# Optimization experiments

Hardware: AMD Instinct MI355X
Metric: run time of the kernel (lower is better)

The kernel has to match this reference:

```python
import jax, jax.numpy as jnp
import numpy as np

N = 8192
IN_F = 512
OUT_F = 512
ALPHA = 0.2
NEG_BIG = -9.0e15


def setup_inputs() -> dict:
    key = jax.random.key(0)
    k1, k2, k3, k4 = jax.random.split(key, 4)
    adjacency = jax.random.randint(k1, (N, N), 0, 2, dtype=jnp.int32)
    features = jax.random.normal(k2, (N, IN_F), dtype=jnp.float32)
    # Linear weight stored as [in, out] (h = x @ W)
    W = jax.random.normal(k3, (IN_F, OUT_F), dtype=jnp.float32) * (1.0 / np.sqrt(IN_F))
    attn = jax.random.normal(k4, (2 * OUT_F, 1), dtype=jnp.float32) * 0.05
    return {"adjacency": adjacency, "features": features, "W": W, "attn": attn}


def reference(adjacency, features, W, attn):
    h = features @ W  # [N, F]
    # Additive decomposition of concat([h_i, h_j]) @ attn:
    # score_ij = a1 . h_i + a2 . h_j  (identical math, no NxNx2F tensor)
    a1 = attn[:OUT_F, 0]  # [F]
    a2 = attn[OUT_F:, 0]  # [F]
    s1 = h @ a1  # [N] contribution of source node i
    s2 = h @ a2  # [N] contribution of target node j
    e = jax.nn.leaky_relu(s1[:, None] + s2[None, :], negative_slope=ALPHA)  # [N, N]
    e = jnp.where(adjacency > 0, e, NEG_BIG)
    attention = jax.nn.softmax(e, axis=1)  # [N, N]
    h_prime = attention @ h  # [N, F]
    return jax.nn.elu(h_prime)
```

## Files before the change

kernel.cpp:

```cpp
#include <hip/hip_runtime.h>
#include <hip/hip_bf16.h>
#include <cstdint>

#define NN 8192
#define F 512
#define LOG2E 1.4426950408889634f

typedef __attribute__((ext_vector_type(8))) short bf16x8;
typedef __attribute__((ext_vector_type(4))) float f32x4;
typedef unsigned int uint32;
typedef unsigned long long u64;
typedef unsigned char uchar;

__device__ __forceinline__ short f2bf(float x){
  __hip_bfloat16 h = __float2bfloat16(x);
  return *reinterpret_cast<short*>(&h);
}

__global__ __launch_bounds__(256) void k_wa(const float* __restrict__ W, const float* __restrict__ attn,
                     float* __restrict__ wa){
  const int lane = threadIdx.x&63, wid = threadIdx.x>>6;
  const int id = blockIdx.x*4 + wid;
  const int b = id>>9, c = id&511;
  const float4* Wr = (const float4*)(W + (size_t)c*F);
  const float4* av = (const float4*)(attn + b*F);
  float s = 0.f;
  #pragma unroll
  for (int h=0;h<2;++h){
    const int k = lane + h*64;
    const float4 wv = Wr[k], a = av[k];
    s += wv.x*a.x + wv.y*a.y + wv.z*a.z + wv.w*a.w;
  }
  for (int off=32;off;off>>=1) s += __shfl_down(s,off);
  if (lane==0) wa[id] = s;
}

__global__ __launch_bounds__(256) void k_tw(const float* __restrict__ W, short* __restrict__ WbT){
  __shared__ short t[64][72];
  const int k0 = blockIdx.x*64, n0 = blockIdx.y*64;
  #pragma unroll
  for (int it=0;it<16;++it){
    const int idx = it*256 + threadIdx.x;
    const int r = idx>>6, c = idx&63;
    t[r][c] = f2bf(W[(size_t)(k0+r)*F + n0 + c]);
  }
  __syncthreads();
  #pragma unroll
  for (int it=0;it<2;++it){
    const int idx = it*256 + threadIdx.x;
    const int n = idx>>3, g = idx&7;
    short v[8];
    #pragma unroll
    for (int e=0;e<8;++e) v[e] = t[g*8+e][n];
    *(uint4*)(WbT + (size_t)(n0+n)*F + k0 + g*8) = *(const uint4*)v;
  }
}

__global__ __launch_bounds__(256) void k_prep(const float* __restrict__ X, const float* __restrict__ wa,
    short* __restrict__ Xb, float2* __restrict__ rowAB, uint32* __restrict__ uwb){
  const int lane = threadIdx.x&63, wid = threadIdx.x>>6;
  const int row = blockIdx.x*4 + wid;
  const float4* X4 = (const float4*)(X + (size_t)row*F);
  const float4* A4 = (const float4*)wa;
  const float4* B4 = (const float4*)(wa + F);
  uint2* Xb4 = (uint2*)(Xb + (size_t)row*F);
  float a1 = 0.f, a2 = 0.f;
  #pragma unroll
  for (int h=0;h<2;++h){
    const int c = lane + h*64;
    const float4 x = X4[c];
    const float4 a = A4[c];
    const float4 b = B4[c];
    a1 += x.x*a.x + x.y*a.y + x.z*a.z + x.w*a.w;
    a2 += x.x*b.x + x.y*b.y + x.z*b.z + x.w*b.w;
    short o[4] = {f2bf(x.x),f2bf(x.y),f2bf(x.z),f2bf(x.w)};
    Xb4[c] = *(const uint2*)o;
  }
  for (int off=32;off;off>>=1){ a1 += __shfl_down(a1,off); a2 += __shfl_down(a2,off); }
  if (lane==0){
    const float s1 = a1*LOG2E, s2 = a2*LOG2E;
    rowAB[row] = make_float2(exp2f(s1), exp2f(0.2f*s1));
    const float u = exp2f(s2), w = exp2f(0.2f*s2);
    uwb[row] = (uint32)(unsigned short)f2bf(u) | ((uint32)(unsigned short)f2bf(w)<<16);
  }
}

__global__ __launch_bounds__(256,2) void k_gemm1(const short* __restrict__ Xb,
    const short* __restrict__ WbT, short* __restrict__ HT){
  __shared__ char smem[33280];
  short* At = (short*)smem;
  short* Bt = (short*)(smem + 16384);
  const int tid=threadIdx.x, lane=tid&63, wid=tid>>6;
  const int m0 = blockIdx.x*128, n0 = blockIdx.y*128;
  f32x4 acc[2][8];
  #pragma unroll
  for (int a=0;a<2;++a)
    #pragma unroll
    for (int b=0;b<8;++b) acc[a][b] = (f32x4){0.f,0.f,0.f,0.f};

  for (int t=0;t<8;++t){
    const int k0 = t*64;
    __syncthreads();
    #pragma unroll
    for (int rnd=0;rnd<4;++rnd){
      const int s = rnd*256 + tid;
      const int n = s>>3, kc = s&7;
      uint4 va = *(const uint4*)(Xb  + (size_t)(m0+n)*F + k0 + kc*8);
      uint4 vb = *(const uint4*)(WbT + (size_t)(n0+n)*F + k0 + kc*8);
      const int off = n*128 + ((kc^(n&7))*16);
      *(uint4*)((char*)At + off) = va;
      *(uint4*)((char*)Bt + off) = vb;
    }
    __syncthreads();
    #pragma unroll
    for (int ks=0;ks<2;++ks){
      const int kc = ks*4 + (lane>>4);
      int r0 = wid*32 + (lane&15);
      int r1 = r0 + 16;
      bf16x8 af0 = *(const bf16x8*)((char*)At + r0*128 + ((kc^(r0&7))*16));
      bf16x8 af1 = *(const bf16x8*)((char*)At + r1*128 + ((kc^(r1&7))*16));
      #pragma unroll
      for (int nf=0;nf<8;++nf){
        const int c = nf*16 + (lane&15);
        bf16x8 bf = *(const bf16x8*)((char*)Bt + c*128 + ((kc^(c&7))*16));
        acc[0][nf] = __builtin_amdgcn_mfma_f32_16x16x32_bf16(af0, bf, acc[0][nf],0,0,0);
        acc[1][nf] = __builtin_amdgcn_mfma_f32_16x16x32_bf16(af1, bf, acc[1][nf],0,0,0);
      }
    }
  }
  __syncthreads();
  short* ct = (short*)smem;
  #pragma unroll
  for (int mf=0;mf<2;++mf)
    #pragma unroll
    for (int nf=0;nf<8;++nf)
      #pragma unroll
      for (int q=0;q<4;++q){
        int r = wid*32 + mf*16 + (lane>>4)*4 + q;
        int c = nf*16 + (lane&15);
        ct[r*130+c] = f2bf(acc[mf][nf][q]);
      }
  __syncthreads();
  {
    const int c = tid>>1, ih0 = (tid&1)*64;
    #pragma unroll
    for (int i8=0;i8<8;++i8){
      short v[8];
      #pragma unroll
      for (int e=0;e<8;++e) v[e] = ct[(ih0+i8*8+e)*130 + c];
      *(uint4*)(HT + (size_t)(n0+c)*NN + m0 + ih0 + i8*8) = *(const uint4*)v;
    }
  }
}

__global__ __launch_bounds__(256,2) void k_pv(const int* __restrict__ adj,
    const short* __restrict__ HT, const uint32* __restrict__ uwb,
    const float2* __restrict__ rowAB, float* __restrict__ Zp,
    float* __restrict__ P0, float* __restrict__ P1,
    float* __restrict__ P2, float* __restrict__ P3, int ksteps){
  __shared__ short Bt2[2][512*32];
  __shared__ short At2[2][64*32];
  __shared__ uint32 uwl[2048];
  const int tid=threadIdx.x, lane=tid&63, wid=tid>>6;
  const int m0 = blockIdx.x*64;
  const int kz = blockIdx.y;
  const int kz0 = kz*(ksteps*32);
  float* const outs[4] = {P0,P1,P2,P3};
  float* outP = outs[kz];

  {
    const uint4* src = (const uint4*)(uwb + kz0);
    uint4 v0 = src[tid], v1 = src[256+tid];
    ((uint4*)uwl)[tid] = v0; ((uint4*)uwl)[256+tid] = v1;
  }

  const int kcs = (tid&3) ^ ((tid>>3)&3);
  const short* gB = HT + (size_t)(tid>>2)*NN + kz0 + kcs*8;

  const int ar = tid>>2, aq = tid&3;
  const float2 E = rowAB[m0 + ar];
  const float A0 = E.x, B0c = E.y;
  const int* adjp = adj + (size_t)(m0+ar)*NN + kz0 + aq*8;
  const int aoff = ar*64 + ((aq ^ ((ar>>1)&3))<<4);

  const int bofs = (((lane>>4) ^ ((lane>>1)&3))<<4);
  const int l15_64 = (lane&15)*64;

  f32x4 acc[4][8];
  #pragma unroll
  for (int i=0;i<4;++i)
    #pragma unroll
    for (int j=0;j<8;++j) acc[i][j] = (f32x4){0.f,0.f,0.f,0.f};
  float zacc = 0.f;

  uint4 b0,b1,b2,b3,b4,b5,b6,b7;
  int4  aA0,aA1, aB0,aB1;

#define PV_BLOAD(tt) { \
    const short* g = gB + (size_t)(tt)*32; \
    b0 = *(const uint4*)(g);               b1 = *(const uint4*)(g + (size_t)1*64*NN); \
    b2 = *(const uint4*)(g + (size_t)2*64*NN); b3 = *(const uint4*)(g + (size_t)3*64*NN); \
    b4 = *(const uint4*)(g + (size_t)4*64*NN); b5 = *(const uint4*)(g + (size_t)5*64*NN); \
    b6 = *(const uint4*)(g + (size_t)6*64*NN); b7 = *(const uint4*)(g + (size_t)7*64*NN); }

#define PV_BWRITE(buf) { \
    uint4* d = (uint4*)(Bt2[buf]); \
    d[      tid] = b0; d[ 256+tid] = b1; d[ 512+tid] = b2; d[ 768+tid] = b3; \
    d[1024+tid] = b4; d[1280+tid] = b5; d[1536+tid] = b6; d[1792+tid] = b7; }

#define PV_ALOAD(r0v,r1v,tt) { \
    r0v = *(const int4*)(adjp + (size_t)(tt)*32); \
    r1v = *(const int4*)(adjp + (size_t)(tt)*32 + 4); }

#define PV_AGEN(abuf, r0v, r1v, tt) { \
    const uint32* uwt = &uwl[(tt)*32 + aq*8]; \
    const uint4 u0 = *(const uint4*)uwt; \
    const uint4 u1 = *(const uint4*)(uwt+4); \
    const uint32 pk[8] = {u0.x,u0.y,u0.z,u0.w,u1.x,u1.y,u1.z,u1.w}; \
    const int    aa[8] = {r0v.x,r0v.y,r0v.z,r0v.w,r1v.x,r1v.y,r1v.z,r1v.w}; \
    short av[8]; \
    _Pragma("unroll") \
    for (int e=0;e<8;++e){ \
      const float u = __uint_as_float(pk[e]<<16); \
      const float w = __uint_as_float(pk[e]&0xffff0000u); \
      float v = fmaxf(A0*u, B0c*w); \
      v = (aa[e] > 0) ? v : 0.f; \
      zacc += v; \
      av[e] = f2bf(v); } \
    *(uint4*)((char*)(At2[abuf]) + aoff) = *(const uint4*)av; }

#define PV_MFMA(buf) { \
    bf16x8 af[4]; \
    _Pragma("unroll") \
    for (int mf=0;mf<4;++mf) \
      af[mf] = *(const bf16x8*)((char*)(At2[buf]) + mf*1024 + l15_64 + bofs); \
    _Pragma("unroll") \
    for (int nf=0;nf<8;++nf){ \
      const bf16x8 bv = *(const bf16x8*)((char*)(Bt2[buf]) + wid*8192 + nf*1024 + l15_64 + bofs); \
      _Pragma("unroll") \
      for (int mf=0;mf<4;++mf) \
        acc[mf][nf] = __builtin_amdgcn_mfma_f32_16x16x32_bf16(af[mf], bv, acc[mf][nf],0,0,0); } }

  PV_ALOAD(aA0,aA1, 0);
  PV_BLOAD(0);
  __syncthreads();
  PV_AGEN(0, aA0,aA1, 0);
  PV_BWRITE(0);
  PV_ALOAD(aB0,aB1, 1);
  __syncthreads();

  for (int t=0; t<ksteps; t+=2){
    {
      if (t+1 < ksteps) PV_BLOAD(t+1);
      if (t+2 < ksteps) PV_ALOAD(aA0,aA1, t+2);
      PV_MFMA(0);
      if (t+1 < ksteps){ PV_AGEN(1, aB0,aB1, t+1); PV_BWRITE(1); }
      __syncthreads();
    }
    if (t+1 < ksteps){
      if (t+2 < ksteps) PV_BLOAD(t+2);
      if (t+3 < ksteps) PV_ALOAD(aB0,aB1, t+3);
      PV_MFMA(1);
      if (t+2 < ksteps){ PV_AGEN(0, aA0,aA1, t+2); PV_BWRITE(0); }
      __syncthreads();
    }
  }

  zacc += __shfl_xor(zacc, 1);
  zacc += __shfl_xor(zacc, 2);
  if (aq == 0) Zp[(size_t)kz*NN + m0 + ar] = zacc;
  #pragma unroll
  for (int mf=0;mf<4;++mf)
    #pragma unroll
    for (int nf=0;nf<8;++nf){
      const int col = wid*128 + nf*16 + (lane&15);
      #pragma unroll
      for (int qq=0;qq<4;++qq){
        const int row = m0 + mf*16 + (lane>>4)*4 + qq;
        outP[(size_t)row*F + col] = acc[mf][nf][qq];
      }
    }
#undef PV_BLOAD
#undef PV_BWRITE
#undef PV_ALOAD
#undef PV_AGEN
#undef PV_MFMA
}

__global__ __launch_bounds__(256) void k_red(const float* __restrict__ P1,
    const float* __restrict__ P2, const float* __restrict__ P3,
    const float* __restrict__ Zp, float* __restrict__ out, int ks){
  const size_t i = ((size_t)blockIdx.x*256 + threadIdx.x)*4;
  const int row = (int)(i >> 9);
  float4 a = *(float4*)(out+i);
  float Z = Zp[row];
  if (ks > 1){
    Z += Zp[NN+row] + Zp[2*NN+row] + Zp[3*NN+row];
    const float4 b1 = *(const float4*)(P1+i);
    const float4 b2 = *(const float4*)(P2+i);
    const float4 b3 = *(const float4*)(P3+i);
    a.x += b1.x+b2.x+b3.x; a.y += b1.y+b2.y+b3.y;
    a.z += b1.z+b2.z+b3.z; a.w += b1.w+b2.w+b3.w;
  }
  const float s = 1.f/Z;
  a.x*=s; a.y*=s; a.z*=s; a.w*=s;
  a.x = (a.x>0.f)?a.x:expm1f(a.x);
  a.y = (a.y>0.f)?a.y:expm1f(a.y);
  a.z = (a.z>0.f)?a.z:expm1f(a.z);
  a.w = (a.w>0.f)?a.w:expm1f(a.w);
  *(float4*)(out+i) = a;
}

extern "C" void kernel_launch(void* const* d_in, const int* in_sizes, int n_in,
                              void* d_out, int out_size, void* d_ws, size_t ws_size,
                              hipStream_t stream) {
  (void)in_sizes; (void)n_in; (void)out_size;
  const int*   adj  = (const int*)d_in[0];
  const float* X    = (const float*)d_in[1];
  const float* W    = (const float*)d_in[2];
  const float* attn = (const float*)d_in[3];
  float* out = (float*)d_out;
  char* ws = (char*)d_ws;
  short*  HT   = (short*)(ws);
  short*  Xb   = (short*)(ws + 8388608);
  short*  WbT  = (short*)(ws + 16777216);
  uint32* uwb  = (uint32*)(ws + 17301504);
  float2* rowAB= (float2*)(ws + 17334272);
  float*  wa   = (float*)(ws + 17399808);
  float*  Zp   = (float*)(ws + 17403904);
  float*  P1   = (float*)(ws + 17534976);
  float*  P2   = (float*)(ws + 34312192);
  float*  P3   = (float*)(ws + 51089408);
  const int KS = (ws_size >= 67866624ull) ? 4 : 1;
  const int ksteps = 256/KS;

  k_wa   <<<dim3(256),    dim3(256), 0, stream>>>(W, attn, wa);
  k_tw   <<<dim3(8,8),    dim3(256), 0, stream>>>(W, WbT);
  k_prep <<<dim3(2048),   dim3(256), 0, stream>>>(X, wa, Xb, rowAB, uwb);
  k_gemm1<<<dim3(64,4),   dim3(256), 0, stream>>>(Xb, WbT, HT);
  k_pv   <<<dim3(128,KS), dim3(256), 0, stream>>>(adj, HT, uwb, rowAB, Zp, out, P1, P2, P3, ksteps);
  k_red  <<<dim3(4096),   dim3(256), 0, stream>>>(P1, P2, P3, Zp, out, KS);
}
```

Measured before the change: 180.3 us.

## Widen k_pv to 512 threads with per-wave 64-column tiles and MFMA priority

Doubles the k_pv workgroup to eight waves, so each wave computes a 64x64 output slice instead of 64x128. This halves per-thread accumulators and B-tile load registers. The adjacency/weight A-tile generation is split across twice as many threads, with 4 elements each, and the per-block LDS copy of uwb is replaced by direct global vector loads. s_setprio is raised around the MFMA block to favour matrix issue over the load and conversion work of other waves. The aggressive launch bound (512,4) may force heavy register limits or spills, and LDS usage still caps residency per CU.

```diff
diff --git a/kernel.cpp b/kernel.cpp
--- a/kernel.cpp
+++ b/kernel.cpp
@@ -153,81 +153,70 @@
   }
 }
 
-__global__ __launch_bounds__(256,2) void k_pv(const int* __restrict__ adj,
+__global__ __launch_bounds__(512,4) void k_pv(const int* __restrict__ adj,
     const short* __restrict__ HT, const uint32* __restrict__ uwb,
     const float2* __restrict__ rowAB, float* __restrict__ Zp,
     float* __restrict__ P0, float* __restrict__ P1,
     float* __restrict__ P2, float* __restrict__ P3, int ksteps){
   __shared__ short Bt2[2][512*32];
   __shared__ short At2[2][64*32];
-  __shared__ uint32 uwl[2048];
-  const int tid=threadIdx.x, lane=tid&63, wid=tid>>6;
+  const int tid=threadIdx.x, lane=tid&63, w=tid>>6;
   const int m0 = blockIdx.x*64;
   const int kz = blockIdx.y;
   const int kz0 = kz*(ksteps*32);
-  float* const outs[4] = {P0,P1,P2,P3};
-  float* outP = outs[kz];
-
-  {
-    const uint4* src = (const uint4*)(uwb + kz0);
-    uint4 v0 = src[tid], v1 = src[256+tid];
-    ((uint4*)uwl)[tid] = v0; ((uint4*)uwl)[256+tid] = v1;
-  }
+  float* outP = (kz==0)?P0:((kz==1)?P1:((kz==2)?P2:P3));
 
   const int kcs = (tid&3) ^ ((tid>>3)&3);
   const short* gB = HT + (size_t)(tid>>2)*NN + kz0 + kcs*8;
 
-  const int ar = tid>>2, aq = tid&3;
+  const int ar = tid>>3, aq = tid&7;
   const float2 E = rowAB[m0 + ar];
   const float A0 = E.x, B0c = E.y;
-  const int* adjp = adj + (size_t)(m0+ar)*NN + kz0 + aq*8;
-  const int aoff = ar*64 + ((aq ^ ((ar>>1)&3))<<4);
+  const int*    adjp = adj + (size_t)(m0+ar)*NN + kz0 + aq*4;
+  const uint32* uwp  = uwb + kz0 + aq*4;
+  const int aoff = ar*64 + ((((aq>>1) ^ ((ar>>1)&3)))<<4) + (aq&1)*8;
 
   const int bofs = (((lane>>4) ^ ((lane>>1)&3))<<4);
   const int l15_64 = (lane&15)*64;
 
-  f32x4 acc[4][8];
+  f32x4 acc[4][4];
   #pragma unroll
   for (int i=0;i<4;++i)
     #pragma unroll
-    for (int j=0;j<8;++j) acc[i][j] = (f32x4){0.f,0.f,0.f,0.f};
+    for (int j=0;j<4;++j) acc[i][j] = (f32x4){0.f,0.f,0.f,0.f};
   float zacc = 0.f;
 
-  uint4 b0,b1,b2,b3,b4,b5,b6,b7;
-  int4  aA0,aA1, aB0,aB1;
+  uint4 b0,b1,b2,b3;
+  int4  aA, aB;
+  uint4 uwr;
 
 #define PV_BLOAD(tt) { \
     const short* g = gB + (size_t)(tt)*32; \
-    b0 = *(const uint4*)(g);               b1 = *(const uint4*)(g + (size_t)1*64*NN); \
-    b2 = *(const uint4*)(g + (size_t)2*64*NN); b3 = *(const uint4*)(g + (size_t)3*64*NN); \
-    b4 = *(const uint4*)(g + (size_t)4*64*NN); b5 = *(const uint4*)(g + (size_t)5*64*NN); \
-    b6 = *(const uint4*)(g + (size_t)6*64*NN); b7 = *(const uint4*)(g + (size_t)7*64*NN); }
+    b0 = *(const uint4*)(g); \
+    b1 = *(const uint4*)(g + (size_t)128*NN); \
+    b2 = *(const uint4*)(g + (size_t)256*NN); \
+    b3 = *(const uint4*)(g + (size_t)384*NN); }
 
 #define PV_BWRITE(buf) { \
     uint4* d = (uint4*)(Bt2[buf]); \
-    d[      tid] = b0; d[ 256+tid] = b1; d[ 512+tid] = b2; d[ 768+tid] = b3; \
-    d[1024+tid] = b4; d[1280+tid] = b5; d[1536+tid] = b6; d[1792+tid] = b7; }
-
-#define PV_ALOAD(r0v,r1v,tt) { \
-    r0v = *(const int4*)(adjp + (size_t)(tt)*32); \
-    r1v = *(const int4*)(adjp + (size_t)(tt)*32 + 4); }
-
-#define PV_AGEN(abuf, r0v, r1v, tt) { \
-    const uint32* uwt = &uwl[(tt)*32 + aq*8]; \
-    const uint4 u0 = *(const uint4*)uwt; \
-    const uint4 u1 = *(const uint4*)(uwt+4); \
-    const uint32 pk[8] = {u0.x,u0.y,u0.z,u0.w,u1.x,u1.y,u1.z,u1.w}; \
-    const int    aa[8] = {r0v.x,r0v.y,r0v.z,r0v.w,r1v.x,r1v.y,r1v.z,r1v.w}; \
-    short av[8]; \
+    d[tid] = b0; d[512+tid] = b1; d[1024+tid] = b2; d[1536+tid] = b3; }
+
+#define PV_ALOAD(dst,tt) { dst = *(const int4*)(adjp + (size_t)(tt)*32); }
+#define PV_ULOAD(tt)     { uwr = *(const uint4*)(uwp + (size_t)(tt)*32); }
+
+#define PV_AGEN(abuf, areg) { \
+    const uint32 pk[4] = {uwr.x,uwr.y,uwr.z,uwr.w}; \
+    const int    aa[4] = {areg.x,areg.y,areg.z,areg.w}; \
+    short av[4]; \
     _Pragma("unroll") \
-    for (int e=0;e<8;++e){ \
+    for (int e=0;e<4;++e){ \
       const float u = __uint_as_float(pk[e]<<16); \
-      const float w = __uint_as_float(pk[e]&0xffff0000u); \
-      float v = fmaxf(A0*u, B0c*w); \
+      const float ww = __uint_as_float(pk[e]&0xffff0000u); \
+      float v = fmaxf(A0*u, B0c*ww); \
       v = (aa[e] > 0) ? v : 0.f; \
       zacc += v; \
       av[e] = f2bf(v); } \
-    *(uint4*)((char*)(At2[abuf]) + aoff) = *(const uint4*)av; }
+    *(uint2*)((char*)(At2[abuf]) + aoff) = *(const uint2*)av; }
 
 #define PV_MFMA(buf) { \
     bf16x8 af[4]; \
@@ -235,54 +224,61 @@
     for (int mf=0;mf<4;++mf) \
       af[mf] = *(const bf16x8*)((char*)(At2[buf]) + mf*1024 + l15_64 + bofs); \
     _Pragma("unroll") \
-    for (int nf=0;nf<8;++nf){ \
-      const bf16x8 bv = *(const bf16x8*)((char*)(Bt2[buf]) + wid*8192 + nf*1024 + l15_64 + bofs); \
+    for (int nf=0;nf<4;++nf){ \
+      const bf16x8 bv = *(const bf16x8*)((char*)(Bt2[buf]) + w*4096 + nf*1024 + l15_64 + bofs); \
       _Pragma("unroll") \
       for (int mf=0;mf<4;++mf) \
         acc[mf][nf] = __builtin_amdgcn_mfma_f32_16x16x32_bf16(af[mf], bv, acc[mf][nf],0,0,0); } }
 
-  PV_ALOAD(aA0,aA1, 0);
+  PV_ALOAD(aA, 0);
+  PV_ULOAD(0);
   PV_BLOAD(0);
-  __syncthreads();
-  PV_AGEN(0, aA0,aA1, 0);
+  PV_AGEN(0, aA);
   PV_BWRITE(0);
-  PV_ALOAD(aB0,aB1, 1);
+  PV_ALOAD(aB, 1);
   __syncthreads();
 
   for (int t=0; t<ksteps; t+=2){
     {
-      if (t+1 < ksteps) PV_BLOAD(t+1);
-      if (t+2 < ksteps) PV_ALOAD(aA0,aA1, t+2);
+      if (t+1 < ksteps){ PV_BLOAD(t+1); PV_ULOAD(t+1); }
+      if (t+2 < ksteps){ PV_ALOAD(aA, t+2); }
+      __builtin_amdgcn_s_setprio(1);
       PV_MFMA(0);
-      if (t+1 < ksteps){ PV_AGEN(1, aB0,aB1, t+1); PV_BWRITE(1); }
+      __builtin_amdgcn_s_setprio(0);
+      if (t+1 < ksteps){ PV_AGEN(1, aB); PV_BWRITE(1); }
       __syncthreads();
     }
     if (t+1 < ksteps){
-      if (t+2 < ksteps) PV_BLOAD(t+2);
-      if (t+3 < ksteps) PV_ALOAD(aB0,aB1, t+3);
+      if (t+2 < ksteps){ PV_BLOAD(t+2); PV_ULOAD(t+2); }
+      if (t+3 < ksteps){ PV_ALOAD(aB, t+3); }
+      __builtin_amdgcn_s_setprio(1);
       PV_MFMA(1);
-      if (t+2 < ksteps){ PV_AGEN(0, aA0,aA1, t+2); PV_BWRITE(0); }
+      __builtin_amdgcn_s_setprio(0);
+      if (t+2 < ksteps){ PV_AGEN(0, aA); PV_BWRITE(0); }
       __syncthreads();
     }
   }
 
   zacc += __shfl_xor(zacc, 1);
   zacc += __shfl_xor(zacc, 2);
+  zacc += __shfl_xor(zacc, 4);
   if (aq == 0) Zp[(size_t)kz*NN + m0 + ar] = zacc;
+
   #pragma unroll
   for (int mf=0;mf<4;++mf)
     #pragma unroll
-    for (int nf=0;nf<8;++nf){
-      const int col = wid*128 + nf*16 + (lane&15);
+    for (int nf=0;nf<4;++nf){
+      const int col = w*64 + nf*16 + (lane&15);
       #pragma unroll
-      for (int qq=0;qq<4;++qq){
-        const int row = m0 + mf*16 + (lane>>4)*4 + qq;
-        outP[(size_t)row*F + col] = acc[mf][nf][qq];
+      for (int q=0;q<4;++q){
+        const int row = m0 + mf*16 + (lane>>4)*4 + q;
+        outP[(size_t)row*F + col] = acc[mf][nf][q];
       }
     }
 #undef PV_BLOAD
 #undef PV_BWRITE
 #undef PV_ALOAD
+#undef PV_ULOAD
 #undef PV_AGEN
 #undef PV_MFMA
 }
@@ -338,6 +334,6 @@
   k_tw   <<<dim3(8,8),    dim3(256), 0, stream>>>(W, WbT);
   k_prep <<<dim3(2048),   dim3(256), 0, stream>>>(X, wa, Xb, rowAB, uwb);
   k_gemm1<<<dim3(64,4),   dim3(256), 0, stream>>>(Xb, WbT, HT);
-  k_pv   <<<dim3(128,KS), dim3(256), 0, stream>>>(adj, HT, uwb, rowAB, Zp, out, P1, P2, P3, ksteps);
+  k_pv   <<<dim3(128,KS), dim3(512), 0, stream>>>(adj, HT, uwb, rowAB, Zp, out, P1, P2, P3, ksteps);
   k_red  <<<dim3(4096),   dim3(256), 0, stream>>>(P1, P2, P3, Zp, out, KS);
 }
```

After: 259.3 us. 1.44x slower.

## Restructure k_pv pipeline with deeper prefetch, custom barriers, and XCD-aware block mapping

Applied to the files above, without the earlier changes.

Reworks the main k_pv loop so that LDS writes and A-tile generation for the next stage come before the MFMAs, with the global loads for the stage after issued earlier. __syncthreads is replaced by an lgkmcnt wait plus s_barrier, and MFMA sections run at raised wave priority. The uwb staging through LDS is dropped in favour of direct global vector loads. Blocks are remapped to a 1D grid that interleaves K-split slices so neighbouring block IDs spread across partitions. This aims to hide global-load latency and barrier stalls, at the cost of more registers and extra global traffic for the uwb values.

```diff
diff --git a/kernel.cpp b/kernel.cpp
--- a/kernel.cpp
+++ b/kernel.cpp
@@ -157,22 +157,19 @@
     const short* __restrict__ HT, const uint32* __restrict__ uwb,
     const float2* __restrict__ rowAB, float* __restrict__ Zp,
     float* __restrict__ P0, float* __restrict__ P1,
-    float* __restrict__ P2, float* __restrict__ P3, int ksteps){
+    float* __restrict__ P2, float* __restrict__ P3, int ksteps, int KS){
   __shared__ short Bt2[2][512*32];
   __shared__ short At2[2][64*32];
-  __shared__ uint32 uwl[2048];
   const int tid=threadIdx.x, lane=tid&63, wid=tid>>6;
-  const int m0 = blockIdx.x*64;
-  const int kz = blockIdx.y;
+  int mx, kz;
+  if (KS == 4){
+    const int id = blockIdx.x;
+    kz = (id&7)>>1;
+    mx = ((id>>3)<<1) + (id&1);
+  } else { kz = 0; mx = blockIdx.x; }
+  const int m0 = mx*64;
   const int kz0 = kz*(ksteps*32);
-  float* const outs[4] = {P0,P1,P2,P3};
-  float* outP = outs[kz];
-
-  {
-    const uint4* src = (const uint4*)(uwb + kz0);
-    uint4 v0 = src[tid], v1 = src[256+tid];
-    ((uint4*)uwl)[tid] = v0; ((uint4*)uwl)[256+tid] = v1;
-  }
+  float* outP = (kz==0)?P0:((kz==1)?P1:((kz==2)?P2:P3));
 
   const int kcs = (tid&3) ^ ((tid>>3)&3);
   const short* gB = HT + (size_t)(tid>>2)*NN + kz0 + kcs*8;
@@ -180,7 +177,8 @@
   const int ar = tid>>2, aq = tid&3;
   const float2 E = rowAB[m0 + ar];
   const float A0 = E.x, B0c = E.y;
-  const int* adjp = adj + (size_t)(m0+ar)*NN + kz0 + aq*8;
+  const int*    adjp = adj + (size_t)(m0+ar)*NN + kz0 + aq*8;
+  const uint32* uwp  = uwb + kz0 + aq*8;
   const int aoff = ar*64 + ((aq ^ ((ar>>1)&3))<<4);
 
   const int bofs = (((lane>>4) ^ ((lane>>1)&3))<<4);
@@ -194,29 +192,29 @@
   float zacc = 0.f;
 
   uint4 b0,b1,b2,b3,b4,b5,b6,b7;
-  int4  aA0,aA1, aB0,aB1;
+  int4  raA0,raA1, raB0,raB1;
+  uint4 ruA0,ruA1, ruB0,ruB1;
 
 #define PV_BLOAD(tt) { \
     const short* g = gB + (size_t)(tt)*32; \
-    b0 = *(const uint4*)(g);               b1 = *(const uint4*)(g + (size_t)1*64*NN); \
+    b0 = *(const uint4*)(g);                   b1 = *(const uint4*)(g + (size_t)1*64*NN); \
     b2 = *(const uint4*)(g + (size_t)2*64*NN); b3 = *(const uint4*)(g + (size_t)3*64*NN); \
     b4 = *(const uint4*)(g + (size_t)4*64*NN); b5 = *(const uint4*)(g + (size_t)5*64*NN); \
     b6 = *(const uint4*)(g + (size_t)6*64*NN); b7 = *(const uint4*)(g + (size_t)7*64*NN); }
 
 #define PV_BWRITE(buf) { \
     uint4* d = (uint4*)(Bt2[buf]); \
-    d[      tid] = b0; d[ 256+tid] = b1; d[ 512+tid] = b2; d[ 768+tid] = b3; \
+    d[     tid] = b0; d[ 256+tid] = b1; d[ 512+tid] = b2; d[ 768+tid] = b3; \
     d[1024+tid] = b4; d[1280+tid] = b5; d[1536+tid] = b6; d[1792+tid] = b7; }
 
-#define PV_ALOAD(r0v,r1v,tt) { \
+#define PV_ALOAD(r0v,r1v,u0v,u1v,tt) { \
     r0v = *(const int4*)(adjp + (size_t)(tt)*32); \
-    r1v = *(const int4*)(adjp + (size_t)(tt)*32 + 4); }
-
-#define PV_AGEN(abuf, r0v, r1v, tt) { \
-    const uint32* uwt = &uwl[(tt)*32 + aq*8]; \
-    const uint4 u0 = *(const uint4*)uwt; \
-    const uint4 u1 = *(const uint4*)(uwt+4); \
-    const uint32 pk[8] = {u0.x,u0.y,u0.z,u0.w,u1.x,u1.y,u1.z,u1.w}; \
+    r1v = *(const int4*)(adjp + (size_t)(tt)*32 + 4); \
+    u0v = *(const uint4*)(uwp + (size_t)(tt)*32); \
+    u1v = *(const uint4*)(uwp + (size_t)(tt)*32 + 4); }
+
+#define PV_AGEN(abuf, r0v,r1v,u0v,u1v) { \
+    const uint32 pk[8] = {u0v.x,u0v.y,u0v.z,u0v.w,u1v.x,u1v.y,u1v.z,u1v.w}; \
     const int    aa[8] = {r0v.x,r0v.y,r0v.z,r0v.w,r1v.x,r1v.y,r1v.z,r1v.w}; \
     short av[8]; \
     _Pragma("unroll") \
@@ -241,29 +239,58 @@
       for (int mf=0;mf<4;++mf) \
         acc[mf][nf] = __builtin_amdgcn_mfma_f32_16x16x32_bf16(af[mf], bv, acc[mf][nf],0,0,0); } }
 
-  PV_ALOAD(aA0,aA1, 0);
+#define PV_BAR() { \
+    asm volatile("s_waitcnt lgkmcnt(0)" ::: "memory"); \
+    __builtin_amdgcn_s_barrier(); \
+    __builtin_amdgcn_sched_barrier(0); }
+
+  PV_ALOAD(raA0,raA1,ruA0,ruA1, 0);
+  PV_ALOAD(raB0,raB1,ruB0,ruB1, 1);
   PV_BLOAD(0);
-  __syncthreads();
-  PV_AGEN(0, aA0,aA1, 0);
+  PV_AGEN(0, raA0,raA1,ruA0,ruA1);
+  PV_ALOAD(raA0,raA1,ruA0,ruA1, 2);
   PV_BWRITE(0);
-  PV_ALOAD(aB0,aB1, 1);
-  __syncthreads();
-
-  for (int t=0; t<ksteps; t+=2){
+  PV_BLOAD(1);
+  PV_BAR();
+
+  for (int t=0; t<ksteps-2; t+=2){
     {
-      if (t+1 < ksteps) PV_BLOAD(t+1);
-      if (t+2 < ksteps) PV_ALOAD(aA0,aA1, t+2);
+      PV_BWRITE(1);
+      PV_AGEN(1, raB0,raB1,ruB0,ruB1);
+      const int tB = t+2;
+      PV_BLOAD(tB);
+      const int tA = (t+3 < ksteps) ? t+3 : 0;
+      PV_ALOAD(raB0,raB1,ruB0,ruB1, tA);
+      __builtin_amdgcn_s_setprio(1);
       PV_MFMA(0);
-      if (t+1 < ksteps){ PV_AGEN(1, aB0,aB1, t+1); PV_BWRITE(1); }
-      __syncthreads();
-    }
-    if (t+1 < ksteps){
-      if (t+2 < ksteps) PV_BLOAD(t+2);
-      if (t+3 < ksteps) PV_ALOAD(aB0,aB1, t+3);
+      __builtin_amdgcn_s_setprio(0);
+      PV_BAR();
+    }
+    {
+      PV_BWRITE(0);
+      PV_AGEN(0, raA0,raA1,ruA0,ruA1);
+      const int tB = (t+3 < ksteps) ? t+3 : 0;
+      PV_BLOAD(tB);
+      const int tA = (t+4 < ksteps) ? t+4 : 0;
+      PV_ALOAD(raA0,raA1,ruA0,ruA1, tA);
+      __builtin_amdgcn_s_setprio(1);
       PV_MFMA(1);
-      if (t+2 < ksteps){ PV_AGEN(0, aA0,aA1, t+2); PV_BWRITE(0); }
-      __syncthreads();
-    }
+      __builtin_amdgcn_s_setprio(0);
+      PV_BAR();
+    }
+  }
+  {
+    PV_BWRITE(1);
+    PV_AGEN(1, raB0,raB1,ruB0,ruB1);
+    __builtin_amdgcn_s_setprio(1);
+    PV_MFMA(0);
+    __builtin_amdgcn_s_setprio(0);
+    PV_BAR();
+  }
+  {
+    __builtin_amdgcn_s_setprio(1);
+    PV_MFMA(1);
+    __builtin_amdgcn_s_setprio(0);
   }
 
   zacc += __shfl_xor(zacc, 1);
@@ -285,6 +312,7 @@
 #undef PV_ALOAD
 #undef PV_AGEN
 #undef PV_MFMA
+#undef PV_BAR
 }
 
 __global__ __launch_bounds__(256) void k_red(const float* __restrict__ P1,
@@ -338,6 +366,6 @@
   k_tw   <<<dim3(8,8),    dim3(256), 0, stream>>>(W, WbT);
   k_prep <<<dim3(2048),   dim3(256), 0, stream>>>(X, wa, Xb, rowAB, uwb);
   k_gemm1<<<dim3(64,4),   dim3(256), 0, stream>>>(Xb, WbT, HT);
-  k_pv   <<<dim3(128,KS), dim3(256), 0, stream>>>(adj, HT, uwb, rowAB, Zp, out, P1, P2, P3, ksteps);
+  k_pv   <<<dim3(128*KS), dim3(256), 0, stream>>>(adj, HT, uwb, rowAB, Zp, out, P1, P2, P3, ksteps, KS);
   k_red  <<<dim3(4096),   dim3(256), 0, stream>>>(P1, P2, P3, Zp, out, KS);
 }
```

Result: slower. 199.5 us (+10.6%).
